# Kernel tuning notes

Hardware: AMD Instinct MI355X
Metric: run time of the kernel (lower is better)

## Reference

```python
import jax, jax.numpy as jnp
import numpy as np

B, T, D, H = 4, 1024, 1024, 16
DK = D // H  # 64
EPS = 1e-5

def setup_inputs() -> dict:
    key = jax.random.key(0)
    ks = jax.random.split(key, 12)
    s = 1.0 / np.sqrt(D)
    return {
        "x": jax.random.normal(ks[0], (B, T, D), jnp.float32),
        "pos_k": jax.random.normal(ks[1], (T, T, DK), jnp.float32),
        "ln_g": jnp.ones((D,), jnp.float32),
        "ln_b": jnp.zeros((D,), jnp.float32),
        "Wq": jax.random.normal(ks[2], (D, D), jnp.float32) * s,
        "bq": jnp.zeros((D,), jnp.float32),
        "Wk": jax.random.normal(ks[3], (D, D), jnp.float32) * s,
        "bk": jnp.zeros((D,), jnp.float32),
        "Wv": jax.random.normal(ks[4], (D, D), jnp.float32) * s,
        "bv": jnp.zeros((D,), jnp.float32),
        "Wo": jax.random.normal(ks[5], (D, D), jnp.float32) * s,
        "bo": jnp.zeros((D,), jnp.float32),
    }

def reference(x, pos_k, ln_g, ln_b, Wq, bq, Wk, bk, Wv, bv, Wo, bo):
    # LayerNorm over last dim
    mu = jnp.mean(x, axis=-1, keepdims=True)
    var = jnp.mean(jnp.square(x - mu), axis=-1, keepdims=True)
    xn = (x - mu) * jax.lax.rsqrt(var + EPS) * ln_g + ln_b
    # Projections -> (B, H, T, DK)
    def proj(W, b):
        return (xn @ W.T + b).reshape(B, T, H, DK).transpose(0, 2, 1, 3)
    q, k, v = proj(Wq, bq), proj(Wk, bk), proj(Wv, bv)
    # Content scores A: (B, H, T, T)
    A = jnp.einsum('bhqd,bhkd->bhqk', q, k)
    # Relative-position bias: pos_k is (Tq, Tk, DK)
    Bb = jnp.einsum('bhqd,qkd->bhqk', q, pos_k)
    scores = (A + Bb) / np.sqrt(DK)
    attn = jax.nn.softmax(scores, axis=-1)
    out = jnp.einsum('bhqk,bhkd->bhqd', attn, v)  # (B, H, T, DK)
    out = out.transpose(0, 2, 1, 3).reshape(B, T, D)
    return out @ Wo.T + bo
```

## Files before the change

### kernel.cpp

```cpp
#include <hip/hip_runtime.h>

#define DEV __device__ __forceinline__

typedef _Float16 f16x8 __attribute__((ext_vector_type(8)));
typedef float f32x4 __attribute__((ext_vector_type(4)));
typedef unsigned short u16;
typedef unsigned int u32;

DEV u16 f2h(float f) { _Float16 h = (_Float16)f; return __builtin_bit_cast(u16, h); }
DEV float h2f(u16 u) { return (float)__builtin_bit_cast(_Float16, u); }

DEV void gl_lds16(const void* g, void* l) {
  __builtin_amdgcn_global_load_lds((__attribute__((address_space(1))) void*)(g),
                                   (__attribute__((address_space(3))) void*)(l), 16, 0, 0);
}

#define MFMA16(a, b, c) __builtin_amdgcn_mfma_f32_16x16x32_f16(a, b, c, 0, 0, 0)

DEV f16x8 lds_frag(const u16* p) { return *reinterpret_cast<const f16x8*>(p); }

__global__ __launch_bounds__(256) void k_ln(const float* __restrict__ x,
                                            const float* __restrict__ g,
                                            const float* __restrict__ b,
                                            u16* __restrict__ xn) {
  const int row = blockIdx.x;
  const int t = threadIdx.x;
  const float4 v = reinterpret_cast<const float4*>(x + (size_t)row * 1024)[t];
  float s = v.x + v.y + v.z + v.w;
  float s2 = v.x * v.x + v.y * v.y + v.z * v.z + v.w * v.w;
#pragma unroll
  for (int m = 1; m < 64; m <<= 1) { s += __shfl_xor(s, m); s2 += __shfl_xor(s2, m); }
  __shared__ float ls[8];
  const int wid = t >> 6, lane = t & 63;
  if (lane == 0) { ls[wid] = s; ls[4 + wid] = s2; }
  __syncthreads();
  s = ls[0] + ls[1] + ls[2] + ls[3];
  s2 = ls[4] + ls[5] + ls[6] + ls[7];
  const float mu = s * (1.0f / 1024.0f);
  const float rs = rsqrtf(s2 * (1.0f / 1024.0f) - mu * mu + 1e-5f);
  const float4 gv = reinterpret_cast<const float4*>(g)[t];
  const float4 bv = reinterpret_cast<const float4*>(b)[t];
  ushort4 o;
  o.x = f2h((v.x - mu) * rs * gv.x + bv.x);
  o.y = f2h((v.y - mu) * rs * gv.y + bv.y);
  o.z = f2h((v.z - mu) * rs * gv.z + bv.z);
  o.w = f2h((v.w - mu) * rs * gv.w + bv.w);
  reinterpret_cast<ushort4*>(xn + (size_t)row * 1024)[t] = o;
}

__global__ __launch_bounds__(256) void k_cvt(const float* __restrict__ wq,
                                             const float* __restrict__ wk,
                                             const float* __restrict__ wv,
                                             const float* __restrict__ wo,
                                             u16* __restrict__ out) {
  const int i = blockIdx.x * 256 + threadIdx.x;
  const int seg = i >> 18;
  const float* src = seg == 0 ? wq : seg == 1 ? wk : seg == 2 ? wv : wo;
  const float4 v = reinterpret_cast<const float4*>(src)[i & 0x3FFFF];
  ushort4 o;
  o.x = f2h(v.x); o.y = f2h(v.y); o.z = f2h(v.z); o.w = f2h(v.w);
  reinterpret_cast<ushort4*>(out)[i] = o;
}

template <int KD>
DEV void gemm_bt_acc(const u16* __restrict__ A, const u16* __restrict__ B,
                     int m0, int n0, u16* As, u16* Bs, f32x4 acc[4][4]) {
  const int t = threadIdx.x;
  const int wid = t >> 6, lane = t & 63;
  const int wr = wid >> 1, wc = wid & 1;
#pragma unroll
  for (int i = 0; i < 4; ++i)
#pragma unroll
    for (int j = 0; j < 4; ++j) acc[i][j] = (f32x4){0.f, 0.f, 0.f, 0.f};
  const int lrow = t >> 2;
  const int lcol = (t & 3) * 8;
  const int fr = lane & 15, fk = (lane >> 4) * 8;
  for (int k0 = 0; k0 < KD; k0 += 32) {
    __syncthreads();
    gl_lds16(A + (size_t)(m0 + lrow) * KD + k0 + lcol, As + wid * 512);
    gl_lds16(A + (size_t)(m0 + 64 + lrow) * KD + k0 + lcol, As + 2048 + wid * 512);
    gl_lds16(B + (size_t)(n0 + lrow) * KD + k0 + lcol, Bs + wid * 512);
    gl_lds16(B + (size_t)(n0 + 64 + lrow) * KD + k0 + lcol, Bs + 2048 + wid * 512);
    __syncthreads();
    f16x8 af[4], bfr[4];
#pragma unroll
    for (int mf = 0; mf < 4; ++mf) af[mf] = lds_frag(As + (wr * 64 + mf * 16 + fr) * 32 + fk);
#pragma unroll
    for (int nf = 0; nf < 4; ++nf) bfr[nf] = lds_frag(Bs + (wc * 64 + nf * 16 + fr) * 32 + fk);
#pragma unroll
    for (int mf = 0; mf < 4; ++mf)
#pragma unroll
      for (int nf = 0; nf < 4; ++nf) acc[mf][nf] = MFMA16(af[mf], bfr[nf], acc[mf][nf]);
  }
}

__global__ __launch_bounds__(256) void k_qkv(const u16* __restrict__ xn, const u16* __restrict__ wcat,
                                             const float* __restrict__ bq, const float* __restrict__ bk,
                                             const float* __restrict__ bv,
                                             u16* __restrict__ Qb, u16* __restrict__ Kb,
                                             u16* __restrict__ VTb) {
  __shared__ u16 As[128 * 32], Bs[128 * 32];
  f32x4 acc[4][4];
  const int m0 = blockIdx.x * 128, n0 = blockIdx.y * 128;
  gemm_bt_acc<1024>(xn, wcat, m0, n0, As, Bs, acc);
  const int t = threadIdx.x;
  const int wid = t >> 6, lane = t & 63;
  const int wr = wid >> 1, wc = wid & 1;
  const int fr = lane & 15, fg = (lane >> 4) * 4;
#pragma unroll
  for (int nf = 0; nf < 4; ++nf) {
    const int n = n0 + wc * 64 + nf * 16 + fr;
    const int which = n >> 10, f = n & 1023, h = f >> 6, dk = f & 63;
    const float biasv = which == 0 ? bq[f] : which == 1 ? bk[f] : bv[f];
#pragma unroll
    for (int mf = 0; mf < 4; ++mf) {
#pragma unroll
      for (int r = 0; r < 4; ++r) {
        const int m = m0 + wr * 64 + mf * 16 + fg + r;
        const int bb = m >> 10, tt = m & 1023;
        const int bh = bb * 16 + h;
        const float v = acc[mf][nf][r] + biasv;
        if (which == 0) {
          Qb[((size_t)bh * 1024 + tt) * 64 + dk] = f2h(v * 0.125f);
        } else if (which == 1) {
          Kb[((size_t)bh * 1024 + tt) * 64 + dk] = f2h(v);
        } else {
          VTb[((size_t)bh * 64 + dk) * 1024 + tt] = f2h(v);
        }
      }
    }
  }
}

__global__ __launch_bounds__(256) void k_bias(const u16* __restrict__ Qb,
                                              const float* __restrict__ pos_k,
                                              u16* __restrict__ biasb) {
  const int q = blockIdx.x;
  __shared__ u16 Qs[64 * 64];
  __shared__ u16 Ps[256 * 64];
  const int t = threadIdx.x;
  const int wid = t >> 6, lane = t & 63;
  const int r8 = t >> 3, c8 = (t & 7) * 8;
  gl_lds16(Qb + ((size_t)r8 * 1024 + q) * 64 + c8, Qs + wid * 512);
  gl_lds16(Qb + ((size_t)(32 + r8) * 1024 + q) * 64 + c8, Qs + 2048 + wid * 512);
  __syncthreads();
  const int fr = lane & 15, fk8 = (lane >> 4) * 8, fg = (lane >> 4) * 4;
  f16x8 qa[4][2];
#pragma unroll
  for (int mf = 0; mf < 4; ++mf)
#pragma unroll
    for (int ks = 0; ks < 2; ++ks)
      qa[mf][ks] = lds_frag(Qs + (mf * 16 + fr) * 64 + ks * 32 + fk8);
  const float4* src = reinterpret_cast<const float4*>(pos_k + (size_t)q * 65536);
  for (int c = 0; c < 4; ++c) {
    __syncthreads();
#pragma unroll
    for (int j = 0; j < 16; ++j) {
      const int g = j * 256 + t;
      const float4 v = src[c * 4096 + g];
      ushort4 o;
      o.x = f2h(v.x); o.y = f2h(v.y); o.z = f2h(v.z); o.w = f2h(v.w);
      *reinterpret_cast<ushort4*>(Ps + g * 4) = o;
    }
    __syncthreads();
    f32x4 acc[4][4];
#pragma unroll
    for (int nf = 0; nf < 4; ++nf) {
      f16x8 pb0 = lds_frag(Ps + (wid * 64 + nf * 16 + fr) * 64 + fk8);
      f16x8 pb1 = lds_frag(Ps + (wid * 64 + nf * 16 + fr) * 64 + 32 + fk8);
#pragma unroll
      for (int mf = 0; mf < 4; ++mf) {
        acc[mf][nf] = (f32x4){0.f, 0.f, 0.f, 0.f};
        acc[mf][nf] = MFMA16(qa[mf][0], pb0, acc[mf][nf]);
        acc[mf][nf] = MFMA16(qa[mf][1], pb1, acc[mf][nf]);
      }
    }
#pragma unroll
    for (int mf = 0; mf < 4; ++mf)
#pragma unroll
      for (int nf = 0; nf < 4; ++nf)
#pragma unroll
        for (int r = 0; r < 4; ++r) {
          const int bh = mf * 16 + fg + r;
          const int k = c * 256 + wid * 64 + nf * 16 + fr;
          biasb[(size_t)bh * 1048576 + (size_t)q * 1024 + k] = f2h(acc[mf][nf][r]);
        }
  }
}

__global__ __launch_bounds__(256) void k_attn(const u16* __restrict__ Qb, const u16* __restrict__ Kb,
                                              const u16* __restrict__ VTb, const u16* __restrict__ biasb,
                                              u16* __restrict__ Ob) {
  const int qt = blockIdx.x, bh = blockIdx.y;
  const int q0 = qt * 64;
  __shared__ u16 Qs[64 * 64], Ks[64 * 64], Vs[64 * 64], Bts[64 * 64];
  __shared__ u16 Psm[4][16 * 64];
  const int t = threadIdx.x;
  const int wid = t >> 6, lane = t & 63;
  const int r8 = t >> 3, c8 = (t & 7) * 8;
  gl_lds16(Qb + ((size_t)bh * 1024 + q0 + r8) * 64 + c8, Qs + wid * 512);
  gl_lds16(Qb + ((size_t)bh * 1024 + q0 + 32 + r8) * 64 + c8, Qs + 2048 + wid * 512);
  __syncthreads();
  const int fr = lane & 15, fk8 = (lane >> 4) * 8, fg = (lane >> 4) * 4;
  f16x8 qa0 = lds_frag(Qs + (wid * 16 + fr) * 64 + fk8);
  f16x8 qa1 = lds_frag(Qs + (wid * 16 + fr) * 64 + 32 + fk8);
  float m_r[4], l_r[4];
  f32x4 oacc[4];
#pragma unroll
  for (int r = 0; r < 4; ++r) { m_r[r] = -1e30f; l_r[r] = 0.f; }
#pragma unroll
  for (int d = 0; d < 4; ++d) oacc[d] = (f32x4){0.f, 0.f, 0.f, 0.f};

  for (int kt = 0; kt < 16; ++kt) {
    const int k0 = kt * 64;
    __syncthreads();
    gl_lds16(Kb + ((size_t)bh * 1024 + k0 + r8) * 64 + c8, Ks + wid * 512);
    gl_lds16(Kb + ((size_t)bh * 1024 + k0 + 32 + r8) * 64 + c8, Ks + 2048 + wid * 512);
    gl_lds16(VTb + ((size_t)bh * 64 + r8) * 1024 + k0 + c8, Vs + wid * 512);
    gl_lds16(VTb + ((size_t)bh * 64 + 32 + r8) * 1024 + k0 + c8, Vs + 2048 + wid * 512);
    gl_lds16(biasb + (size_t)bh * 1048576 + (size_t)(q0 + r8) * 1024 + k0 + c8, Bts + wid * 512);
    gl_lds16(biasb + (size_t)bh * 1048576 + (size_t)(q0 + 32 + r8) * 1024 + k0 + c8,
             Bts + 2048 + wid * 512);
    __syncthreads();
    f32x4 s[4];
#pragma unroll
    for (int nf = 0; nf < 4; ++nf) {
      f32x4 c0;
#pragma unroll
      for (int r = 0; r < 4; ++r) c0[r] = h2f(Bts[(wid * 16 + fg + r) * 64 + nf * 16 + fr]);
      f16x8 kf0 = lds_frag(Ks + (nf * 16 + fr) * 64 + fk8);
      f16x8 kf1 = lds_frag(Ks + (nf * 16 + fr) * 64 + 32 + fk8);
      c0 = MFMA16(qa0, kf0, c0);
      c0 = MFMA16(qa1, kf1, c0);
      s[nf] = c0;
    }
    float scale_old[4], psum[4];
#pragma unroll
    for (int r = 0; r < 4; ++r) {
      float v = fmaxf(fmaxf(s[0][r], s[1][r]), fmaxf(s[2][r], s[3][r]));
      v = fmaxf(v, __shfl_xor(v, 1));
      v = fmaxf(v, __shfl_xor(v, 2));
      v = fmaxf(v, __shfl_xor(v, 4));
      v = fmaxf(v, __shfl_xor(v, 8));
      const float mn = fmaxf(m_r[r], v);
      scale_old[r] = __expf(m_r[r] - mn);
      m_r[r] = mn;
      psum[r] = 0.f;
    }
#pragma unroll
    for (int nf = 0; nf < 4; ++nf) {
#pragma unroll
      for (int r = 0; r < 4; ++r) {
        const float p = __expf(s[nf][r] - m_r[r]);
        psum[r] += p;
        Psm[wid][(fg + r) * 64 + nf * 16 + fr] = f2h(p);
      }
    }
#pragma unroll
    for (int r = 0; r < 4; ++r) {
      float v = psum[r];
      v += __shfl_xor(v, 1); v += __shfl_xor(v, 2);
      v += __shfl_xor(v, 4); v += __shfl_xor(v, 8);
      l_r[r] = l_r[r] * scale_old[r] + v;
    }
#pragma unroll
    for (int d = 0; d < 4; ++d)
#pragma unroll
      for (int r = 0; r < 4; ++r) oacc[d][r] *= scale_old[r];
    f16x8 pa0 = lds_frag(&Psm[wid][fr * 64 + fk8]);
    f16x8 pa1 = lds_frag(&Psm[wid][fr * 64 + 32 + fk8]);
#pragma unroll
    for (int d = 0; d < 4; ++d) {
      f16x8 vf0 = lds_frag(Vs + (d * 16 + fr) * 64 + fk8);
      f16x8 vf1 = lds_frag(Vs + (d * 16 + fr) * 64 + 32 + fk8);
      oacc[d] = MFMA16(pa0, vf0, oacc[d]);
      oacc[d] = MFMA16(pa1, vf1, oacc[d]);
    }
  }
  const int b_ = bh >> 4, h = bh & 15;
#pragma unroll
  for (int r = 0; r < 4; ++r) {
    const float inv = 1.0f / l_r[r];
    const int tq = q0 + wid * 16 + fg + r;
#pragma unroll
    for (int d = 0; d < 4; ++d)
      Ob[((size_t)b_ * 1024 + tq) * 1024 + h * 64 + d * 16 + fr] = f2h(oacc[d][r] * inv);
  }
}

__global__ __launch_bounds__(256) void k_out(const u16* __restrict__ Ob, const u16* __restrict__ wo,
                                             const float* __restrict__ bo, float* __restrict__ out) {
  __shared__ u16 As[128 * 32], Bs[128 * 32];
  f32x4 acc[4][4];
  const int m0 = blockIdx.x * 128, n0 = blockIdx.y * 128;
  gemm_bt_acc<1024>(Ob, wo, m0, n0, As, Bs, acc);
  const int t = threadIdx.x;
  const int wid = t >> 6, lane = t & 63;
  const int wr = wid >> 1, wc = wid & 1;
  const int fr = lane & 15, fg = (lane >> 4) * 4;
#pragma unroll
  for (int nf = 0; nf < 4; ++nf) {
    const int n = n0 + wc * 64 + nf * 16 + fr;
    const float biasv = bo[n];
#pragma unroll
    for (int mf = 0; mf < 4; ++mf)
#pragma unroll
      for (int r = 0; r < 4; ++r) {
        const int m = m0 + wr * 64 + mf * 16 + fg + r;
        out[(size_t)m * 1024 + n] = acc[mf][nf][r] + biasv;
      }
  }
}

extern "C" void kernel_launch(void* const* d_in, const int* in_sizes, int n_in,
                              void* d_out, int out_size, void* d_ws, size_t ws_size,
                              hipStream_t stream) {
  (void)in_sizes; (void)n_in; (void)out_size; (void)ws_size;
  const float* x     = (const float*)d_in[0];
  const float* pos_k = (const float*)d_in[1];
  const float* ln_g  = (const float*)d_in[2];
  const float* ln_b  = (const float*)d_in[3];
  const float* Wq    = (const float*)d_in[4];
  const float* bq    = (const float*)d_in[5];
  const float* Wk    = (const float*)d_in[6];
  const float* bk    = (const float*)d_in[7];
  const float* Wv    = (const float*)d_in[8];
  const float* bv    = (const float*)d_in[9];
  const float* Wo    = (const float*)d_in[10];
  const float* bo    = (const float*)d_in[11];
  float* out = (float*)d_out;
  char* ws = (char*)d_ws;
  u16* xn    = (u16*)(ws);
  u16* wcat  = (u16*)(ws + (8u << 20));
  u16* wo_h  = (u16*)(ws + (14u << 20));
  u16* Qb    = (u16*)(ws + (16u << 20));
  u16* Kb    = (u16*)(ws + (24u << 20));
  u16* VTb   = (u16*)(ws + (32u << 20));
  u16* Ob    = (u16*)(ws + (40u << 20));
  u16* biasb = (u16*)(ws + (48u << 20));

  k_ln<<<4096, 256, 0, stream>>>(x, ln_g, ln_b, xn);
  k_cvt<<<4096, 256, 0, stream>>>(Wq, Wk, Wv, Wo, wcat);
  k_qkv<<<dim3(32, 24), 256, 0, stream>>>(xn, wcat, bq, bk, bv, Qb, Kb, VTb);
  k_bias<<<1024, 256, 0, stream>>>(Qb, pos_k, biasb);
  k_attn<<<dim3(16, 64), 256, 0, stream>>>(Qb, Kb, VTb, biasb, Ob);
  k_out<<<dim3(32, 8), 256, 0, stream>>>(Ob, wo_h, bo, out);
}
```

Measured before the change: 263.9 us.

## Store Q/K/V/bias in pre-swizzled 64x64 tiles and remap block order

Q, K, V^T and the position bias are now written in 64x64 tile-contiguous layouts with an XOR swizzle, so attention tile loads become contiguous 8KB copies and LDS fragment reads avoid bank conflicts. k_bias drops its LDS staging of pos_k and loads fp32 fragments straight into registers, converting them to fp16 for the MFMA. Both k_bias and k_attn remap block indices, likely to spread work across XCDs and improve L2 locality. The risk is that the uncoalesced direct global loads in k_bias cost more than the LDS staging they replace.

Measured after the change: 279.9 us. +6.1%, slower.

```diff
diff --git a/kernel.cpp b/kernel.cpp
--- a/kernel.cpp
+++ b/kernel.cpp
@@ -18,6 +18,8 @@
 #define MFMA16(a, b, c) __builtin_amdgcn_mfma_f32_16x16x32_f16(a, b, c, 0, 0, 0)
 
 DEV f16x8 lds_frag(const u16* p) { return *reinterpret_cast<const f16x8*>(p); }
+
+DEV int swz(int row, int col) { return (row * 64 + col) ^ ((row & 7) << 3); }
 
 __global__ __launch_bounds__(256) void k_ln(const float* __restrict__ x,
                                             const float* __restrict__ g,
@@ -119,13 +121,15 @@
         const int m = m0 + wr * 64 + mf * 16 + fg + r;
         const int bb = m >> 10, tt = m & 1023;
         const int bh = bb * 16 + h;
+        const int tile = tt >> 6, tr = tt & 63;
+        const size_t base = (size_t)bh * 65536 + tile * 4096;
         const float v = acc[mf][nf][r] + biasv;
         if (which == 0) {
-          Qb[((size_t)bh * 1024 + tt) * 64 + dk] = f2h(v * 0.125f);
+          Qb[base + swz(tr, dk)] = f2h(v * 0.125f);
         } else if (which == 1) {
-          Kb[((size_t)bh * 1024 + tt) * 64 + dk] = f2h(v);
+          Kb[base + swz(tr, dk)] = f2h(v);
         } else {
-          VTb[((size_t)bh * 64 + dk) * 1024 + tt] = f2h(v);
+          VTb[base + swz(dk, tr)] = f2h(v);
         }
       }
     }
@@ -135,14 +139,17 @@
 __global__ __launch_bounds__(256) void k_bias(const u16* __restrict__ Qb,
                                               const float* __restrict__ pos_k,
                                               u16* __restrict__ biasb) {
-  const int q = blockIdx.x;
+  const int q = (blockIdx.x & 7) * 128 + (blockIdx.x >> 3);
+  const int qt = q >> 6, qr = q & 63;
   __shared__ u16 Qs[64 * 64];
-  __shared__ u16 Ps[256 * 64];
   const int t = threadIdx.x;
   const int wid = t >> 6, lane = t & 63;
   const int r8 = t >> 3, c8 = (t & 7) * 8;
-  gl_lds16(Qb + ((size_t)r8 * 1024 + q) * 64 + c8, Qs + wid * 512);
-  gl_lds16(Qb + ((size_t)(32 + r8) * 1024 + q) * 64 + c8, Qs + 2048 + wid * 512);
+  {
+    const size_t qoff = (size_t)qt * 4096 + swz(qr, c8);
+    gl_lds16(Qb + (size_t)r8 * 65536 + qoff, Qs + wid * 512);
+    gl_lds16(Qb + (size_t)(32 + r8) * 65536 + qoff, Qs + 2048 + wid * 512);
+  }
   __syncthreads();
   const int fr = lane & 15, fk8 = (lane >> 4) * 8, fg = (lane >> 4) * 4;
   f16x8 qa[4][2];
@@ -151,30 +158,34 @@
 #pragma unroll
     for (int ks = 0; ks < 2; ++ks)
       qa[mf][ks] = lds_frag(Qs + (mf * 16 + fr) * 64 + ks * 32 + fk8);
-  const float4* src = reinterpret_cast<const float4*>(pos_k + (size_t)q * 65536);
+  const float* pq = pos_k + (size_t)q * 65536;
   for (int c = 0; c < 4; ++c) {
-    __syncthreads();
-#pragma unroll
-    for (int j = 0; j < 16; ++j) {
-      const int g = j * 256 + t;
-      const float4 v = src[c * 4096 + g];
-      ushort4 o;
-      o.x = f2h(v.x); o.y = f2h(v.y); o.z = f2h(v.z); o.w = f2h(v.w);
-      *reinterpret_cast<ushort4*>(Ps + g * 4) = o;
-    }
-    __syncthreads();
+    const int k0 = c * 256 + wid * 64;
+    const int kt = c * 4 + wid;
     f32x4 acc[4][4];
 #pragma unroll
+    for (int i = 0; i < 4; ++i)
+#pragma unroll
+      for (int j = 0; j < 4; ++j) acc[i][j] = (f32x4){0.f, 0.f, 0.f, 0.f};
+#pragma unroll
     for (int nf = 0; nf < 4; ++nf) {
-      f16x8 pb0 = lds_frag(Ps + (wid * 64 + nf * 16 + fr) * 64 + fk8);
-      f16x8 pb1 = lds_frag(Ps + (wid * 64 + nf * 16 + fr) * 64 + 32 + fk8);
+      const float* row = pq + (size_t)(k0 + nf * 16 + fr) * 64;
+      const float4 v0 = *reinterpret_cast<const float4*>(row + fk8);
+      const float4 v1 = *reinterpret_cast<const float4*>(row + fk8 + 4);
+      const float4 v2 = *reinterpret_cast<const float4*>(row + 32 + fk8);
+      const float4 v3 = *reinterpret_cast<const float4*>(row + 32 + fk8 + 4);
+      f16x8 b0, b1;
+      b0[0] = (_Float16)v0.x; b0[1] = (_Float16)v0.y; b0[2] = (_Float16)v0.z; b0[3] = (_Float16)v0.w;
+      b0[4] = (_Float16)v1.x; b0[5] = (_Float16)v1.y; b0[6] = (_Float16)v1.z; b0[7] = (_Float16)v1.w;
+      b1[0] = (_Float16)v2.x; b1[1] = (_Float16)v2.y; b1[2] = (_Float16)v2.z; b1[3] = (_Float16)v2.w;
+      b1[4] = (_Float16)v3.x; b1[5] = (_Float16)v3.y; b1[6] = (_Float16)v3.z; b1[7] = (_Float16)v3.w;
 #pragma unroll
       for (int mf = 0; mf < 4; ++mf) {
-        acc[mf][nf] = (f32x4){0.f, 0.f, 0.f, 0.f};
-        acc[mf][nf] = MFMA16(qa[mf][0], pb0, acc[mf][nf]);
-        acc[mf][nf] = MFMA16(qa[mf][1], pb1, acc[mf][nf]);
+        acc[mf][nf] = MFMA16(qa[mf][0], b0, acc[mf][nf]);
+        acc[mf][nf] = MFMA16(qa[mf][1], b1, acc[mf][nf]);
       }
     }
+    u16* dst = biasb + (size_t)qt * 65536 + (size_t)kt * 4096;
 #pragma unroll
     for (int mf = 0; mf < 4; ++mf)
 #pragma unroll
@@ -182,8 +193,8 @@
 #pragma unroll
         for (int r = 0; r < 4; ++r) {
           const int bh = mf * 16 + fg + r;
-          const int k = c * 256 + wid * 64 + nf * 16 + fr;
-          biasb[(size_t)bh * 1048576 + (size_t)q * 1024 + k] = f2h(acc[mf][nf][r]);
+          const int kr = nf * 16 + fr;
+          dst[(size_t)bh * 1048576 + swz(qr, kr)] = f2h(acc[mf][nf][r]);
         }
   }
 }
@@ -191,19 +202,19 @@
 __global__ __launch_bounds__(256) void k_attn(const u16* __restrict__ Qb, const u16* __restrict__ Kb,
                                               const u16* __restrict__ VTb, const u16* __restrict__ biasb,
                                               u16* __restrict__ Ob) {
-  const int qt = blockIdx.x, bh = blockIdx.y;
+  const int idx = (blockIdx.x & 7) * 128 + (blockIdx.x >> 3);
+  const int qt = idx & 15, bh = idx >> 4;
   const int q0 = qt * 64;
   __shared__ u16 Qs[64 * 64], Ks[64 * 64], Vs[64 * 64], Bts[64 * 64];
   __shared__ u16 Psm[4][16 * 64];
   const int t = threadIdx.x;
   const int wid = t >> 6, lane = t & 63;
-  const int r8 = t >> 3, c8 = (t & 7) * 8;
-  gl_lds16(Qb + ((size_t)bh * 1024 + q0 + r8) * 64 + c8, Qs + wid * 512);
-  gl_lds16(Qb + ((size_t)bh * 1024 + q0 + 32 + r8) * 64 + c8, Qs + 2048 + wid * 512);
+  gl_lds16(Qb + (size_t)bh * 65536 + qt * 4096 + t * 8, Qs + wid * 512);
+  gl_lds16(Qb + (size_t)bh * 65536 + qt * 4096 + 2048 + t * 8, Qs + 2048 + wid * 512);
   __syncthreads();
   const int fr = lane & 15, fk8 = (lane >> 4) * 8, fg = (lane >> 4) * 4;
-  f16x8 qa0 = lds_frag(Qs + (wid * 16 + fr) * 64 + fk8);
-  f16x8 qa1 = lds_frag(Qs + (wid * 16 + fr) * 64 + 32 + fk8);
+  f16x8 qa0 = lds_frag(Qs + swz(wid * 16 + fr, fk8));
+  f16x8 qa1 = lds_frag(Qs + swz(wid * 16 + fr, 32 + fk8));
   float m_r[4], l_r[4];
   f32x4 oacc[4];
 #pragma unroll
@@ -211,25 +222,27 @@
 #pragma unroll
   for (int d = 0; d < 4; ++d) oacc[d] = (f32x4){0.f, 0.f, 0.f, 0.f};
 
+  const u16* Kbase = Kb + (size_t)bh * 65536;
+  const u16* Vbase = VTb + (size_t)bh * 65536;
+  const u16* Bbase = biasb + (size_t)bh * 1048576 + (size_t)qt * 65536;
+
   for (int kt = 0; kt < 16; ++kt) {
-    const int k0 = kt * 64;
     __syncthreads();
-    gl_lds16(Kb + ((size_t)bh * 1024 + k0 + r8) * 64 + c8, Ks + wid * 512);
-    gl_lds16(Kb + ((size_t)bh * 1024 + k0 + 32 + r8) * 64 + c8, Ks + 2048 + wid * 512);
-    gl_lds16(VTb + ((size_t)bh * 64 + r8) * 1024 + k0 + c8, Vs + wid * 512);
-    gl_lds16(VTb + ((size_t)bh * 64 + 32 + r8) * 1024 + k0 + c8, Vs + 2048 + wid * 512);
-    gl_lds16(biasb + (size_t)bh * 1048576 + (size_t)(q0 + r8) * 1024 + k0 + c8, Bts + wid * 512);
-    gl_lds16(biasb + (size_t)bh * 1048576 + (size_t)(q0 + 32 + r8) * 1024 + k0 + c8,
-             Bts + 2048 + wid * 512);
+    gl_lds16(Kbase + kt * 4096 + t * 8, Ks + wid * 512);
+    gl_lds16(Kbase + kt * 4096 + 2048 + t * 8, Ks + 2048 + wid * 512);
+    gl_lds16(Vbase + kt * 4096 + t * 8, Vs + wid * 512);
+    gl_lds16(Vbase + kt * 4096 + 2048 + t * 8, Vs + 2048 + wid * 512);
+    gl_lds16(Bbase + kt * 4096 + t * 8, Bts + wid * 512);
+    gl_lds16(Bbase + kt * 4096 + 2048 + t * 8, Bts + 2048 + wid * 512);
     __syncthreads();
     f32x4 s[4];
 #pragma unroll
     for (int nf = 0; nf < 4; ++nf) {
       f32x4 c0;
 #pragma unroll
-      for (int r = 0; r < 4; ++r) c0[r] = h2f(Bts[(wid * 16 + fg + r) * 64 + nf * 16 + fr]);
-      f16x8 kf0 = lds_frag(Ks + (nf * 16 + fr) * 64 + fk8);
-      f16x8 kf1 = lds_frag(Ks + (nf * 16 + fr) * 64 + 32 + fk8);
+      for (int r = 0; r < 4; ++r) c0[r] = h2f(Bts[swz(wid * 16 + fg + r, nf * 16 + fr)]);
+      f16x8 kf0 = lds_frag(Ks + swz(nf * 16 + fr, fk8));
+      f16x8 kf1 = lds_frag(Ks + swz(nf * 16 + fr, 32 + fk8));
       c0 = MFMA16(qa0, kf0, c0);
       c0 = MFMA16(qa1, kf1, c0);
       s[nf] = c0;
@@ -253,7 +266,7 @@
       for (int r = 0; r < 4; ++r) {
         const float p = __expf(s[nf][r] - m_r[r]);
         psum[r] += p;
-        Psm[wid][(fg + r) * 64 + nf * 16 + fr] = f2h(p);
+        Psm[wid][swz(fg + r, nf * 16 + fr) & 1023] = f2h(p);
       }
     }
 #pragma unroll
@@ -267,12 +280,12 @@
     for (int d = 0; d < 4; ++d)
 #pragma unroll
       for (int r = 0; r < 4; ++r) oacc[d][r] *= scale_old[r];
-    f16x8 pa0 = lds_frag(&Psm[wid][fr * 64 + fk8]);
-    f16x8 pa1 = lds_frag(&Psm[wid][fr * 64 + 32 + fk8]);
+    f16x8 pa0 = lds_frag(&Psm[wid][swz(fr, fk8) & 1023]);
+    f16x8 pa1 = lds_frag(&Psm[wid][swz(fr, 32 + fk8) & 1023]);
 #pragma unroll
     for (int d = 0; d < 4; ++d) {
-      f16x8 vf0 = lds_frag(Vs + (d * 16 + fr) * 64 + fk8);
-      f16x8 vf1 = lds_frag(Vs + (d * 16 + fr) * 64 + 32 + fk8);
+      f16x8 vf0 = lds_frag(Vs + swz(d * 16 + fr, fk8));
+      f16x8 vf1 = lds_frag(Vs + swz(d * 16 + fr, 32 + fk8));
       oacc[d] = MFMA16(pa0, vf0, oacc[d]);
       oacc[d] = MFMA16(pa1, vf1, oacc[d]);
     }
@@ -343,6 +356,6 @@
   k_cvt<<<4096, 256, 0, stream>>>(Wq, Wk, Wv, Wo, wcat);
   k_qkv<<<dim3(32, 24), 256, 0, stream>>>(xn, wcat, bq, bk, bv, Qb, Kb, VTb);
   k_bias<<<1024, 256, 0, stream>>>(Qb, pos_k, biasb);
-  k_attn<<<dim3(16, 64), 256, 0, stream>>>(Qb, Kb, VTb, biasb, Ob);
+  k_attn<<<dim3(1024), 256, 0, stream>>>(Qb, Kb, VTb, biasb, Ob);
   k_out<<<dim3(32, 8), 256, 0, stream>>>(Ob, wo_h, bo, out);
 }
```
